# Optimization experiments

Hardware: AMD Instinct MI355X
Metric: run time of the kernel (lower is better)

The kernel has to match this reference:

```python
import jax, jax.numpy as jnp
import numpy as np

HEAD = 8
SCALE = 0.17677669529663687  # 1/sqrt(32)

def setup_inputs() -> dict:
    key = jax.random.key(0)
    ks = jax.random.split(key, 6)
    N, S, R, M, Z = 1, 128, 256, 256, 128
    return {
        "msa_repr": jax.random.normal(ks[0], (N, S, R, M), jnp.float32),
        "pair_repr": jax.random.normal(ks[1], (N, R, R, Z), jnp.float32),
        "gate_proj": jax.random.normal(ks[2], (M, M), jnp.float32) * 0.02,
        "qkv_proj": jax.random.normal(ks[3], (M, 3 * M), jnp.float32) * 0.02,
        "out_proj": jax.random.normal(ks[4], (M, M), jnp.float32) * 0.02,
        "bias_proj": jax.random.normal(ks[5], (Z, HEAD), jnp.float32) * 0.02,
    }

def reference(msa_repr, pair_repr, gate_proj, qkv_proj, out_proj, bias_proj):
    N, S, R, M = msa_repr.shape
    h = HEAD
    c = M // h
    # pair bias: [N,R,R,Z] @ [Z,h] -> [N,h,R,R]
    bias = jnp.einsum('nrpz,zh->nhrp', pair_repr, bias_proj)
    # gated QKV projections
    gate = jax.nn.sigmoid(msa_repr @ gate_proj).reshape(N, S, R, h, c)
    qkv = (msa_repr @ qkv_proj).reshape(N, S, R, h, 3 * c)
    q, k, v = jnp.split(qkv, 3, axis=-1)  # each [N,S,R,h,c]
    # attention over rows (R): sim [N,S,h,R,R]
    sim = jnp.einsum('nsrhc,nsphc->nshrp', q, k) * SCALE
    probs = jax.nn.softmax(sim, axis=-1)
    # NOTE: bias is added AFTER softmax (faithful to original)
    probs = probs + bias[:, None, :, :, :]
    attend = jnp.einsum('nshrp,nsphc->nsrhc', probs, v) * gate
    out = attend.reshape(N, S, R, M) @ out_proj
    return out
```

## Files before the change

kernel.cpp:

```cpp
#include <hip/hip_runtime.h>
#include <hip/hip_bf16.h>
#include <math.h>

typedef __attribute__((ext_vector_type(8))) short bf16x8;
typedef __attribute__((ext_vector_type(4))) short bf16x4;
typedef __attribute__((ext_vector_type(4))) float f32x4;

#define MFMA32 __builtin_amdgcn_mfma_f32_16x16x32_bf16
#define MFMA16 __builtin_amdgcn_mfma_f32_16x16x16bf16_1k

#define QSCALE 0.25503485964546277f

__device__ inline short bfbits(float f) {
  union { float f; unsigned u; } v; v.f = f;
  unsigned r = v.u + 0x7fffu + ((v.u >> 16) & 1u);
  return (short)(r >> 16);
}
__device__ inline float bf2f(unsigned short u) {
  union { unsigned u; float f; } v; v.u = ((unsigned)u) << 16; return v.f;
}
__device__ inline void gll16(const void* g, void* l) {
  __builtin_amdgcn_global_load_lds(
      (const __attribute__((address_space(1))) unsigned*)g,
      (__attribute__((address_space(3))) unsigned*)l, 16, 0, 0);
}
__device__ inline bf16x4 pk4(float e0, float e1, float e2, float e3) {
  unsigned lo, hi;
  asm("v_cvt_pk_bf16_f32 %0, %1, %2" : "=v"(lo) : "v"(e0), "v"(e1));
  asm("v_cvt_pk_bf16_f32 %0, %1, %2" : "=v"(hi) : "v"(e2), "v"(e3));
  union { unsigned u[2]; bf16x4 v; } cv;
  cv.u[0] = lo; cv.u[1] = hi;
  return cv.v;
}

__global__ __launch_bounds__(256) void prep2_kernel(
    const float* __restrict__ X, const float* __restrict__ pair,
    const float* __restrict__ bproj, const float* __restrict__ Wg,
    const float* __restrict__ Wqkv, const float* __restrict__ Wout,
    short* __restrict__ Xbf, short* __restrict__ bias_bf,
    short* __restrict__ Wh, short* __restrict__ Woutt) {
  __shared__ float bp[1024];
  __shared__ float red[128][8];
  int bid = blockIdx.x;
  int t = threadIdx.x;
  if (bid < 512) {
    for (int i = t; i < 1024; i += 256)
      bp[i] = bproj[(i & 127) * 8 + (i >> 7)];
    __syncthreads();
    int row = bid * 128 + (t & 127);
    int zh = t >> 7;
    const float4* src = (const float4*)(pair + (size_t)row * 128 + zh * 64);
    float acc[8] = {};
#pragma unroll
    for (int z4 = 0; z4 < 16; ++z4) {
      float4 v = src[z4];
#pragma unroll
      for (int h = 0; h < 8; ++h) {
        float4 b = *(const float4*)&bp[h * 128 + zh * 64 + z4 * 4];
        acc[h] += v.x * b.x + v.y * b.y + v.z * b.z + v.w * b.w;
      }
    }
    if (t >= 128) {
#pragma unroll
      for (int h = 0; h < 8; ++h) red[t - 128][h] = acc[h];
    }
    __syncthreads();
    if (t < 128) {
#pragma unroll
      for (int h = 0; h < 8; ++h)
        bias_bf[(size_t)h * 65536 + row] = bfbits(acc[h] + red[t][h]);
    }
  } else if (bid < 1792) {
    int idx = (bid - 512) * 256 + t;
    if (idx < 262144) {
      int h = idx >> 15, rem = idx & 32767;
      int c = rem >> 8, k = rem & 255;
      float v;
      if (c < 96) {
        v = Wqkv[k * 768 + h * 96 + c];
        if (c < 32) v *= QSCALE;
      } else {
        v = Wg[k * 256 + h * 32 + (c - 96)];
      }
      Wh[idx] = bfbits(v);
    } else {
      int j = idx - 262144;
      int col = j >> 8, k = j & 255;
      Woutt[j] = bfbits(Wout[k * 256 + col]);
    }
  } else {
    size_t i = ((size_t)(bid - 1792) * 256 + t) * 8;
    float4 a = *(const float4*)(X + i);
    float4 b = *(const float4*)(X + i + 4);
    bf16x8 o = {bfbits(a.x), bfbits(a.y), bfbits(a.z), bfbits(a.w),
                bfbits(b.x), bfbits(b.y), bfbits(b.z), bfbits(b.w)};
    *(bf16x8*)(Xbf + i) = o;
  }
}

__global__ __launch_bounds__(512, 4) void fused_qkvattn(
    const short* __restrict__ Xbf, const short* __restrict__ Wh,
    const short* __restrict__ bias_bf, short* __restrict__ attn_bf) {
  __shared__ short lds[33024];
  int t = threadIdx.x;
  int lane = t & 63, wid = t >> 6;
  int lq = lane & 15, lg = lane >> 4;
  int flat = blockIdx.x;
  int xcd = flat & 7, local = flat >> 3;
  int h = local & 7;
  int s = xcd * 16 + (local >> 3);

  const short* xrow0 = Xbf + (size_t)s * 65536;
  const short* whh = Wh + h * 32768;

  int wm = wid >> 1, wn = wid & 1;
  auto stageA = [&](int kq, int buf) {
#pragma unroll
    for (int c = 0; c < 2; ++c) {
      int D = c * 8192 + t * 16;
      int row = D >> 6;
      int sl = ((D >> 4) & 3) ^ ((row >> 1) & 3);
      gll16(xrow0 + (size_t)row * 256 + kq * 32 + sl * 8,
            (char*)lds + buf * 16384 + D);
    }
  };
  auto stageB = [&](int kq, int buf) {
    int D = t * 16;
    int col = D >> 6;
    int sl = ((D >> 4) & 3) ^ ((col >> 1) & 3);
    gll16(whh + (size_t)col * 256 + kq * 32 + sl * 8,
          (char*)lds + 32768 + buf * 8192 + D);
  };

  f32x4 acc[4][4];
#pragma unroll
  for (int a = 0; a < 4; ++a)
#pragma unroll
    for (int b = 0; b < 4; ++b) acc[a][b] = {0.f, 0.f, 0.f, 0.f};

  stageA(0, 0);
  stageB(0, 0);
  __syncthreads();

  for (int kq = 0; kq < 8; ++kq) {
    int buf = kq & 1;
    if (kq < 7) {
      stageA(kq + 1, buf ^ 1);
      stageB(kq + 1, buf ^ 1);
    }
    bf16x8 afr[4], bfr[4];
#pragma unroll
    for (int mf = 0; mf < 4; ++mf) {
      int row = wm * 64 + mf * 16 + lq;
      int sl = lg ^ ((row >> 1) & 3);
      afr[mf] = *(const bf16x8*)((const char*)lds + buf * 16384 + row * 64 +
                                 sl * 16);
    }
#pragma unroll
    for (int nf = 0; nf < 4; ++nf) {
      int col = wn * 64 + nf * 16 + lq;
      int sl = lg ^ ((col >> 1) & 3);
      bfr[nf] = *(const bf16x8*)((const char*)lds + 32768 + buf * 8192 +
                                 col * 64 + sl * 16);
    }
#pragma unroll
    for (int mf = 0; mf < 4; ++mf)
#pragma unroll
      for (int nf = 0; nf < 4; ++nf)
        acc[mf][nf] = MFMA32(afr[mf], bfr[nf], acc[mf][nf], 0, 0, 0);
    __syncthreads();
  }

  short* Ks = lds;
  short* Qs = lds + 8192;
  short* Vt = lds + 16384;
  short* Gs = lds + 24704;
  if (wn == 0) {
#pragma unroll
    for (int mf = 0; mf < 4; ++mf)
#pragma unroll
      for (int nf = 0; nf < 4; ++nf) {
        int c = nf * 16 + lq;
        int cc = c & 31;
        char* base = (char*)lds + ((c < 32) ? 16384 : 0);
#pragma unroll
        for (int j = 0; j < 4; ++j) {
          int R = wm * 64 + mf * 16 + lg * 4 + j;
          *(short*)(base + R * 64 + ((((cc >> 3) ^ ((R >> 1) & 3)) << 4)) +
                    (cc & 7) * 2) = bfbits(acc[mf][nf][j]);
        }
      }
  } else {
#pragma unroll
    for (int mf = 0; mf < 4; ++mf)
#pragma unroll
      for (int nf = 0; nf < 4; ++nf) {
        int R0 = wm * 64 + mf * 16 + lg * 4;
        if (nf < 2) {
          int c = nf * 16 + lq;
          bf16x4 v4 = {bfbits(acc[mf][nf][0]), bfbits(acc[mf][nf][1]),
                       bfbits(acc[mf][nf][2]), bfbits(acc[mf][nf][3])};
          *(bf16x4*)&Vt[c * 260 + R0] = v4;
        } else {
          int c = (nf - 2) * 16 + lq;
          bf16x4 g4;
#pragma unroll
          for (int j = 0; j < 4; ++j)
            g4[j] = bfbits(
                __builtin_amdgcn_rcpf(1.f + __expf(-acc[mf][nf][j])));
          *(bf16x4*)&Gs[c * 260 + R0] = g4;
        }
      }
  }
  __syncthreads();

  int rbase = wid * 32;
  int qrow0 = rbase + lq, qrow1 = rbase + 16 + lq;
  bf16x8 qf0 = *(const bf16x8*)((const char*)lds + 16384 + qrow0 * 64 +
                                ((lg ^ ((qrow0 >> 1) & 3)) << 4));
  bf16x8 qf1 = *(const bf16x8*)((const char*)lds + 16384 + qrow1 * 64 +
                                ((lg ^ ((qrow1 >> 1) & 3)) << 4));
  const short* bb0 =
      bias_bf + ((size_t)h * 256 + rbase + lq) * 256 + lg * 8;
  const short* bb1 = bb0 + 16 * 256;

  f32x4 U[2][2], BV[2][2], L[2];
#pragma unroll
  for (int ri = 0; ri < 2; ++ri) {
    L[ri] = {0.f, 0.f, 0.f, 0.f};
#pragma unroll
    for (int ct = 0; ct < 2; ++ct) {
      U[ri][ct] = {0.f, 0.f, 0.f, 0.f};
      BV[ri][ct] = {0.f, 0.f, 0.f, 0.f};
    }
  }
  const bf16x4 ones = {16256, 16256, 16256, 16256};

#pragma unroll
  for (int qtr = 0; qtr < 4; ++qtr) {
    f32x4 sim[2][4];
#pragma unroll
    for (int ri = 0; ri < 2; ++ri)
#pragma unroll
      for (int i = 0; i < 4; ++i) sim[ri][i] = {0.f, 0.f, 0.f, 0.f};
    __builtin_amdgcn_s_setprio(1);
#pragma unroll
    for (int i = 0; i < 4; ++i) {
      int row = (qtr * 4 + i) * 16 + lq;
      bf16x8 kf = *(const bf16x8*)((const char*)lds + row * 64 +
                                   ((lg ^ ((row >> 1) & 3)) << 4));
      sim[0][i] = MFMA32(kf, qf0, sim[0][i], 0, 0, 0);
      sim[1][i] = MFMA32(kf, qf1, sim[1][i], 0, 0, 0);
    }
#pragma unroll
    for (int c2 = 0; c2 < 2; ++c2) {
      int chunk = qtr * 2 + c2;
      bf16x8 b0 = *(const bf16x8*)(bb0 + chunk * 32);
      bf16x8 b1 = *(const bf16x8*)(bb1 + chunk * 32);
      bf16x8 v0 = *(const bf16x8*)&Vt[lq * 260 + chunk * 32 + lg * 8];
      bf16x8 v1 = *(const bf16x8*)&Vt[(16 + lq) * 260 + chunk * 32 + lg * 8];
      BV[0][0] = MFMA32(b0, v0, BV[0][0], 0, 0, 0);
      BV[0][1] = MFMA32(b0, v1, BV[0][1], 0, 0, 0);
      BV[1][0] = MFMA32(b1, v0, BV[1][0], 0, 0, 0);
      BV[1][1] = MFMA32(b1, v1, BV[1][1], 0, 0, 0);
    }
    __builtin_amdgcn_s_setprio(0);

    bf16x4 af[2][4];
#pragma unroll
    for (int ri = 0; ri < 2; ++ri)
#pragma unroll
      for (int i = 0; i < 4; ++i)
        af[ri][i] = pk4(__builtin_amdgcn_exp2f(sim[ri][i][0]),
                        __builtin_amdgcn_exp2f(sim[ri][i][1]),
                        __builtin_amdgcn_exp2f(sim[ri][i][2]),
                        __builtin_amdgcn_exp2f(sim[ri][i][3]));

    __builtin_amdgcn_s_setprio(1);
#pragma unroll
    for (int i = 0; i < 4; ++i) {
      int kc = qtr * 4 + i;
      bf16x4 vf0 = *(const bf16x4*)&Vt[lq * 260 + kc * 16 + lg * 4];
      bf16x4 vf1 = *(const bf16x4*)&Vt[(16 + lq) * 260 + kc * 16 + lg * 4];
#pragma unroll
      for (int ri = 0; ri < 2; ++ri) {
        U[ri][0] = MFMA16(af[ri][i], vf0, U[ri][0], 0, 0, 0);
        U[ri][1] = MFMA16(af[ri][i], vf1, U[ri][1], 0, 0, 0);
        L[ri]    = MFMA16(af[ri][i], ones, L[ri], 0, 0, 0);
      }
    }
    __builtin_amdgcn_s_setprio(0);
  }

  __syncthreads();
  short* Res = Ks;

#pragma unroll
  for (int ri = 0; ri < 2; ++ri) {
    f32x4 inv;
#pragma unroll
    for (int j = 0; j < 4; ++j) inv[j] = __builtin_amdgcn_rcpf(L[ri][j]);
#pragma unroll
    for (int ct = 0; ct < 2; ++ct) {
      int c = ct * 16 + lq;
      bf16x4 g4 = *(const bf16x4*)&Gs[c * 260 + rbase + ri * 16 + lg * 4];
#pragma unroll
      for (int j = 0; j < 4; ++j) {
        int rl = rbase + ri * 16 + lg * 4 + j;
        Res[rl * 32 + c] =
            bfbits((U[ri][ct][j] * inv[j] + BV[ri][ct][j]) *
                   bf2f((unsigned short)g4[j]));
      }
    }
  }
  __syncthreads();

  {
    int row = t >> 1, hf = t & 1;
    size_t o = ((size_t)(s * 256 + row)) * 256 + h * 32 + hf * 16;
    bf16x8 r0 = *(const bf16x8*)&Res[row * 32 + hf * 16];
    bf16x8 r1 = *(const bf16x8*)&Res[row * 32 + hf * 16 + 8];
    *(bf16x8*)&attn_bf[o] = r0;
    *(bf16x8*)&attn_bf[o + 8] = r1;
  }
}

__global__ __launch_bounds__(256) void gemm_out2(
    const short* __restrict__ A, const short* __restrict__ Wt,
    float* __restrict__ out) {
  __shared__ short As2[2][128 * 64];
  __shared__ short Bs2[2][128 * 64];
  int t = threadIdx.x;
  int lane = t & 63, wid = t >> 6;
  int lq = lane & 15, lg = lane >> 4;
  int wm = wid >> 1, wn = wid & 1;
  int r0 = blockIdx.x * 128, n0 = blockIdx.y * 128;

  auto stage = [&](int s, int buf) {
#pragma unroll
    for (int q = 0; q < 4; ++q) {
      int P = wid * 4096 + q * 1024 + lane * 16;
      int row = P >> 7, kb = P & 127;
      int klog = kb ^ ((row & 7) << 4);
      gll16((const char*)A + ((size_t)(r0 + row) * 512 + s * 128 + klog),
            (char*)&As2[buf][0] + wid * 4096 + q * 1024);
      gll16((const char*)Wt + ((size_t)(n0 + row) * 512 + s * 128 + klog),
            (char*)&Bs2[buf][0] + wid * 4096 + q * 1024);
    }
  };

  f32x4 acc[4][4];
#pragma unroll
  for (int a = 0; a < 4; ++a)
#pragma unroll
    for (int b = 0; b < 4; ++b) acc[a][b] = {0.f, 0.f, 0.f, 0.f};

  stage(0, 0);
  __syncthreads();
  for (int s = 0; s < 4; ++s) {
    if (s < 3) stage(s + 1, (s + 1) & 1);
    bf16x8 afr[4][2], bfr[4][2];
#pragma unroll
    for (int kcl = 0; kcl < 2; ++kcl) {
#pragma unroll
      for (int mf = 0; mf < 4; ++mf) {
        int row = wm * 64 + mf * 16 + lq;
        int kb = (((kcl << 6) | (lg << 4))) ^ ((row & 7) << 4);
        afr[mf][kcl] = *(const bf16x8*)((const char*)&As2[s & 1][0] + row * 128 + kb);
      }
#pragma unroll
      for (int nf = 0; nf < 4; ++nf) {
        int col = wn * 64 + nf * 16 + lq;
        int kb = (((kcl << 6) | (lg << 4))) ^ ((col & 7) << 4);
        bfr[nf][kcl] = *(const bf16x8*)((const char*)&Bs2[s & 1][0] + col * 128 + kb);
      }
    }
#pragma unroll
    for (int mf = 0; mf < 4; ++mf)
#pragma unroll
      for (int nf = 0; nf < 4; ++nf)
#pragma unroll
        for (int kcl = 0; kcl < 2; ++kcl)
          acc[mf][nf] = MFMA32(afr[mf][kcl], bfr[nf][kcl], acc[mf][nf], 0, 0, 0);
    __syncthreads();
  }
#pragma unroll
  for (int mf = 0; mf < 4; ++mf)
#pragma unroll
    for (int nf = 0; nf < 4; ++nf) {
      int col = n0 + wn * 64 + nf * 16 + lq;
#pragma unroll
      for (int j = 0; j < 4; ++j) {
        int row = r0 + wm * 64 + mf * 16 + lg * 4 + j;
        out[(size_t)row * 256 + col] = acc[mf][nf][j];
      }
    }
}

extern "C" void kernel_launch(void* const* d_in, const int* in_sizes, int n_in,
                              void* d_out, int out_size, void* d_ws,
                              size_t ws_size, hipStream_t stream) {
  const float* msa  = (const float*)d_in[0];
  const float* pair = (const float*)d_in[1];
  const float* Wg   = (const float*)d_in[2];
  const float* Wqkv = (const float*)d_in[3];
  const float* Wout = (const float*)d_in[4];
  const float* Bp   = (const float*)d_in[5];
  float* out = (float*)d_out;
  short* sw = (short*)d_ws;

  short* bias_bf = sw;
  short* attn_bf = sw + 524288;
  short* Wh_bf   = sw + 8912896;
  short* Woutt   = sw + 9175040;
  short* X_bf    = sw + 9240576;

  hipLaunchKernelGGL(prep2_kernel, dim3(5888), dim3(256), 0, stream,
                     msa, pair, Bp, Wg, Wqkv, Wout,
                     X_bf, bias_bf, Wh_bf, Woutt);
  hipLaunchKernelGGL(fused_qkvattn, dim3(1024), dim3(512), 0, stream,
                     X_bf, Wh_bf, bias_bf, attn_bf);
  hipLaunchKernelGGL(gemm_out2, dim3(256, 2), dim3(256), 0, stream,
                     attn_bf, Woutt, out);
}
```

Before: 76.57 us.

## Transpose K/Q accumulator stores, stagger key quarters per wave, head-major attn output

For the K/Q half, the projection GEMM now computes the transposed product by swapping MFMA operands. Each lane can then write four contiguous bf16 values as one vector store instead of four scalar stores into the swizzled LDS tiles. The attention loop starts each wave at a different key quarter, which spreads LDS bank and bias-load contention across waves. The attention output moves to a head-major layout so each block writes one contiguous region, and the output GEMM's A-loader is changed to read that layout. The risk is less coalesced global loads in the output GEMM, since each 16-byte load now draws from per-head planes.

```diff
diff --git a/kernel.cpp b/kernel.cpp
--- a/kernel.cpp
+++ b/kernel.cpp
@@ -163,16 +163,22 @@
       bfr[nf] = *(const bf16x8*)((const char*)lds + 32768 + buf * 8192 +
                                  col * 64 + sl * 16);
     }
-#pragma unroll
-    for (int mf = 0; mf < 4; ++mf)
-#pragma unroll
-      for (int nf = 0; nf < 4; ++nf)
-        acc[mf][nf] = MFMA32(afr[mf], bfr[nf], acc[mf][nf], 0, 0, 0);
+    if (wn == 0) {
+#pragma unroll
+      for (int mf = 0; mf < 4; ++mf)
+#pragma unroll
+        for (int nf = 0; nf < 4; ++nf)
+          acc[mf][nf] = MFMA32(bfr[nf], afr[mf], acc[mf][nf], 0, 0, 0);
+    } else {
+#pragma unroll
+      for (int mf = 0; mf < 4; ++mf)
+#pragma unroll
+        for (int nf = 0; nf < 4; ++nf)
+          acc[mf][nf] = MFMA32(afr[mf], bfr[nf], acc[mf][nf], 0, 0, 0);
+    }
     __syncthreads();
   }
 
-  short* Ks = lds;
-  short* Qs = lds + 8192;
   short* Vt = lds + 16384;
   short* Gs = lds + 24704;
   if (wn == 0) {
@@ -180,15 +186,14 @@
     for (int mf = 0; mf < 4; ++mf)
 #pragma unroll
       for (int nf = 0; nf < 4; ++nf) {
-        int c = nf * 16 + lq;
-        int cc = c & 31;
-        char* base = (char*)lds + ((c < 32) ? 16384 : 0);
-#pragma unroll
-        for (int j = 0; j < 4; ++j) {
-          int R = wm * 64 + mf * 16 + lg * 4 + j;
-          *(short*)(base + R * 64 + ((((cc >> 3) ^ ((R >> 1) & 3)) << 4)) +
-                    (cc & 7) * 2) = bfbits(acc[mf][nf][j]);
-        }
+        int p = wm * 64 + mf * 16 + lq;
+        int c0 = nf * 16 + lg * 4;
+        int cc0 = c0 & 31;
+        char* base = (char*)lds + ((nf < 2) ? 16384 : 0);
+        int slot = (cc0 >> 3) ^ ((p >> 1) & 3);
+        bf16x4 pk = {bfbits(acc[mf][nf][0]), bfbits(acc[mf][nf][1]),
+                     bfbits(acc[mf][nf][2]), bfbits(acc[mf][nf][3])};
+        *(bf16x4*)(base + p * 64 + slot * 16 + ((cc0 & 7) * 2)) = pk;
       }
   } else {
 #pragma unroll
@@ -237,7 +242,8 @@
   const bf16x4 ones = {16256, 16256, 16256, 16256};
 
 #pragma unroll
-  for (int qtr = 0; qtr < 4; ++qtr) {
+  for (int qq = 0; qq < 4; ++qq) {
+    int qtr = (qq + (wid & 3)) & 3;
     f32x4 sim[2][4];
 #pragma unroll
     for (int ri = 0; ri < 2; ++ri)
@@ -293,7 +299,7 @@
   }
 
   __syncthreads();
-  short* Res = Ks;
+  short* Res = lds;
 
 #pragma unroll
   for (int ri = 0; ri < 2; ++ri) {
@@ -317,7 +323,7 @@
 
   {
     int row = t >> 1, hf = t & 1;
-    size_t o = ((size_t)(s * 256 + row)) * 256 + h * 32 + hf * 16;
+    size_t o = (size_t)h * 1048576 + ((size_t)(s * 256 + row)) * 32 + hf * 16;
     bf16x8 r0 = *(const bf16x8*)&Res[row * 32 + hf * 16];
     bf16x8 r1 = *(const bf16x8*)&Res[row * 32 + hf * 16 + 8];
     *(bf16x8*)&attn_bf[o] = r0;
@@ -342,7 +348,9 @@
       int P = wid * 4096 + q * 1024 + lane * 16;
       int row = P >> 7, kb = P & 127;
       int klog = kb ^ ((row & 7) << 4);
-      gll16((const char*)A + ((size_t)(r0 + row) * 512 + s * 128 + klog),
+      int kel = s * 64 + (klog >> 1);
+      gll16(A + ((size_t)(kel >> 5) * 1048576 +
+                 (size_t)(r0 + row) * 32 + (kel & 31)),
             (char*)&As2[buf][0] + wid * 4096 + q * 1024);
       gll16((const char*)Wt + ((size_t)(n0 + row) * 512 + s * 128 + klog),
             (char*)&Bs2[buf][0] + wid * 4096 + q * 1024);
```

New measurement: 176.1 us. 130% more time.
